# Performance work log

Measured on AMD Instinct MI355X. Metric: run time of the kernel, lower is better.

## Reference

```python
import jax, jax.numpy as jnp
import numpy as np

D_MODEL = 256
NUM_HEAD = 4
D_HEAD = D_MODEL // NUM_HEAD
B, N, M = 1, 512, 512


def setup_inputs() -> dict:
    key = jax.random.key(0)
    ks = jax.random.split(key, 13)
    s = 1.0 / np.sqrt(D_MODEL)
    inp = {
        'input_q': jax.random.normal(ks[0], (B, N, D_MODEL), jnp.float32),
        'input_k': jax.random.normal(ks[1], (B, M, D_MODEL), jnp.float32),
        'input_v': jax.random.normal(ks[2], (B, M, D_MODEL), jnp.float32),
        'input_p': jax.random.normal(ks[3], (B, N, M, D_MODEL), jnp.float32),
        'key_masks': jnp.zeros((B, M), dtype=bool),
        'Wq': jax.random.normal(ks[4], (D_MODEL, D_MODEL), jnp.float32) * s,
        'bq': jnp.zeros((D_MODEL,), jnp.float32),
        'Wk': jax.random.normal(ks[5], (D_MODEL, D_MODEL), jnp.float32) * s,
        'bk': jnp.zeros((D_MODEL,), jnp.float32),
        'Wv': jax.random.normal(ks[6], (D_MODEL, D_MODEL), jnp.float32) * s,
        'bv': jnp.zeros((D_MODEL,), jnp.float32),
        'Wp': jax.random.normal(ks[7], (D_MODEL, D_MODEL), jnp.float32) * s,
        'bp': jnp.zeros((D_MODEL,), jnp.float32),
    }
    return inp


def reference(input_q, input_k, input_v, input_p, key_masks,
              Wq, bq, Wk, bk, Wv, bv, Wp, bp):
    H, Dh = NUM_HEAD, D_HEAD
    b, n, _ = input_q.shape
    m = input_k.shape[1]
    # linear projections (PyTorch Linear: x @ W.T + b)
    q = (input_q @ Wq.T + bq).reshape(b, n, H, Dh).transpose(0, 2, 1, 3)   # (B,H,N,Dh)
    k = (input_k @ Wk.T + bk).reshape(b, m, H, Dh).transpose(0, 2, 1, 3)   # (B,H,M,Dh)
    v = (input_v @ Wv.T + bv).reshape(b, m, H, Dh).transpose(0, 2, 1, 3)   # (B,H,M,Dh)
    p = (input_p @ Wp.T + bp).reshape(b, n, m, H, Dh)                      # (B,N,M,H,Dh)
    # content scores + per-pair RPE scores (q dot p)
    scores = (jnp.einsum('bhnd,bhmd->bhnm', q, k)
              + jnp.einsum('bhnd,bnmhd->bhnm', q, p)) / np.sqrt(Dh)
    scores = jnp.where(key_masks[:, None, None, :], -jnp.inf, scores)
    attn = jax.nn.softmax(scores, axis=-1)                                 # (B,H,N,M)
    hidden = jnp.einsum('bhnm,bhmd->bhnd', attn, v)
    hidden = hidden.transpose(0, 2, 1, 3).reshape(b, n, H * Dh)            # (B,N,C)
    return hidden
```

## Files before the change

### kernel.cpp

```cpp
#include <hip/hip_runtime.h>
#include <math.h>

#define DMODEL 256
#define NSEQ   512
#define MSEQ   512
#define NHEAD  4
#define DHEAD  64

#define WS_Q      0
#define WS_K      131072
#define WS_V      262144
#define WS_WPE    393216
#define WS_SCORES 917504

__global__ __launch_bounds__(256) void proj_qkv(
    const float* __restrict__ xq, const float* __restrict__ xk,
    const float* __restrict__ xv,
    const float* __restrict__ Wq, const float* __restrict__ bq,
    const float* __restrict__ Wk, const float* __restrict__ bk,
    const float* __restrict__ Wv, const float* __restrict__ bv,
    float* __restrict__ ws)
{
    int bid = blockIdx.x;
    int mat = bid >> 6;
    int rb  = bid & 63;
    const float* X; const float* W; const float* b; float* Y;
    if (mat == 0)      { X = xq; W = Wq; b = bq; Y = ws + WS_Q; }
    else if (mat == 1) { X = xk; W = Wk; b = bk; Y = ws + WS_K; }
    else               { X = xv; W = Wv; b = bv; Y = ws + WS_V; }

    int c  = threadIdx.x;
    int r0 = rb * 8;
    float acc[8];
    float bias = b[c];
#pragma unroll
    for (int r = 0; r < 8; ++r) acc[r] = bias;

    const float4* Wrow = (const float4*)(W + (size_t)c * DMODEL);
    for (int d4 = 0; d4 < 64; ++d4) {
        float4 w = Wrow[d4];
#pragma unroll
        for (int r = 0; r < 8; ++r) {
            float4 x = ((const float4*)(X + (size_t)(r0 + r) * DMODEL))[d4];
            acc[r] += w.x * x.x + w.y * x.y + w.z * x.z + w.w * x.w;
        }
    }
#pragma unroll
    for (int r = 0; r < 8; ++r)
        Y[(size_t)(r0 + r) * DMODEL + c] = acc[r];
}

__global__ __launch_bounds__(256) void make_wpeff(
    const float* __restrict__ Wp, float* __restrict__ ws)
{
    const float* q   = ws + WS_Q;
    float*       wpe = ws + WS_WPE;
    int n0 = blockIdx.x * 2;
    int d  = threadIdx.x;

    const float* q0 = q + (size_t)n0 * DMODEL;
    const float* q1 = q0 + DMODEL;

    float acc0[4] = {0.f, 0.f, 0.f, 0.f};
    float acc1[4] = {0.f, 0.f, 0.f, 0.f};
#pragma unroll
    for (int h = 0; h < 4; ++h) {
        for (int dh = 0; dh < 64; ++dh) {
            int c = h * 64 + dh;
            float w = Wp[(size_t)c * DMODEL + d];
            acc0[h] += q0[c] * w;
            acc1[h] += q1[c] * w;
        }
    }
    *(float4*)&wpe[(size_t)n0 * 1024 + d * 4] =
        make_float4(acc0[0], acc0[1], acc0[2], acc0[3]);
    *(float4*)&wpe[(size_t)(n0 + 1) * 1024 + d * 4] =
        make_float4(acc1[0], acc1[1], acc1[2], acc1[3]);
}

__global__ __launch_bounds__(256) void p_scores(
    const float* __restrict__ Xp, float* __restrict__ ws)
{
    const float* wpe    = ws + WS_WPE;
    float*       scores = ws + WS_SCORES;

    int bid  = blockIdx.x;
    int n    = bid >> 1;
    int half = bid & 1;
    int m    = half * 256 + threadIdx.x;

    __shared__ float4 wl[256];
    wl[threadIdx.x] = ((const float4*)(wpe + (size_t)n * 1024))[threadIdx.x];
    __syncthreads();

    const float4* xrow =
        (const float4*)(Xp + (size_t)((size_t)n * MSEQ + m) * DMODEL);
    float4 acc = make_float4(0.f, 0.f, 0.f, 0.f);
#pragma unroll 8
    for (int d4 = 0; d4 < 64; ++d4) {
        float4 x  = xrow[d4];
        float4 w0 = wl[d4 * 4 + 0];
        float4 w1 = wl[d4 * 4 + 1];
        float4 w2 = wl[d4 * 4 + 2];
        float4 w3 = wl[d4 * 4 + 3];
        acc.x += x.x * w0.x + x.y * w1.x + x.z * w2.x + x.w * w3.x;
        acc.y += x.x * w0.y + x.y * w1.y + x.z * w2.y + x.w * w3.y;
        acc.z += x.x * w0.z + x.y * w1.z + x.z * w2.z + x.w * w3.z;
        acc.w += x.x * w0.w + x.y * w1.w + x.z * w2.w + x.w * w3.w;
    }
    size_t base = (size_t)n * MSEQ + m;
    scores[0 * 262144 + base] = acc.x;
    scores[1 * 262144 + base] = acc.y;
    scores[2 * 262144 + base] = acc.z;
    scores[3 * 262144 + base] = acc.w;
}

__global__ __launch_bounds__(256) void qk_scores(
    const float* __restrict__ bp, float* __restrict__ ws)
{
    const float* q      = ws + WS_Q;
    const float* k      = ws + WS_K;
    float*       scores = ws + WS_SCORES;

    int bid = blockIdx.x;
    int h   = bid >> 6;
    int nt  = (bid >> 3) & 7;
    int mt  = bid & 7;
    int n0  = nt * 64, m0 = mt * 64;

    __shared__ float qs[64][76];
    __shared__ float ks[64][76];
    __shared__ float qb[64];

    int tid = threadIdx.x;
#pragma unroll
    for (int rep = 0; rep < 4; ++rep) {
        int idx = rep * 1024 + tid * 4;
        int row = idx >> 6, col = idx & 63;
        *(float4*)&qs[row][col] =
            *(const float4*)&q[(size_t)(n0 + row) * DMODEL + h * 64 + col];
        *(float4*)&ks[row][col] =
            *(const float4*)&k[(size_t)(m0 + row) * DMODEL + h * 64 + col];
    }
    __syncthreads();

    if (tid < 64) {
        float s = 0.f;
        for (int dh = 0; dh < 64; ++dh) s += qs[tid][dh] * bp[h * 64 + dh];
        qb[tid] = s;
    }
    __syncthreads();

    int tn = tid >> 4, tm = tid & 15;
    float acc[4][4] = {};
    for (int kk = 0; kk < 64; kk += 4) {
        float4 qf[4], kf[4];
#pragma unroll
        for (int i = 0; i < 4; ++i) {
            qf[i] = *(const float4*)&qs[tn * 4 + i][kk];
            kf[i] = *(const float4*)&ks[tm * 4 + i][kk];
        }
#pragma unroll
        for (int i = 0; i < 4; ++i)
#pragma unroll
            for (int j = 0; j < 4; ++j)
                acc[i][j] += qf[i].x * kf[j].x + qf[i].y * kf[j].y +
                             qf[i].z * kf[j].z + qf[i].w * kf[j].w;
    }

#pragma unroll
    for (int i = 0; i < 4; ++i) {
        int n = n0 + tn * 4 + i;
        float qbn = qb[tn * 4 + i];
        float4* p = (float4*)&scores[(size_t)h * 262144 +
                                     (size_t)n * MSEQ + m0 + tm * 4];
        float4 sp = *p;
        sp.x = 0.125f * (sp.x + acc[i][0] + qbn);
        sp.y = 0.125f * (sp.y + acc[i][1] + qbn);
        sp.z = 0.125f * (sp.z + acc[i][2] + qbn);
        sp.w = 0.125f * (sp.w + acc[i][3] + qbn);
        *p = sp;
    }
}

__global__ __launch_bounds__(256) void softmax_av(
    const unsigned char* __restrict__ mask,
    float* __restrict__ out, float* __restrict__ ws)
{
    const float* v      = ws + WS_V;
    const float* scores = ws + WS_SCORES;

    int bid = blockIdx.x;
    int h   = bid >> 6;
    int g   = bid & 63;
    int n0  = g * 8;

    __shared__ float  pl[MSEQ * 8];
    __shared__ float4 red4[256];
    __shared__ float  wred[4];

    int tid  = threadIdx.x;
    int lane = tid & 63, wv = tid >> 6;

    for (int j = 0; j < 8; ++j) {
        int n = n0 + j;
        const float* srow = scores + (size_t)h * 262144 + (size_t)n * MSEQ;
        float s0 = srow[tid];
        float s1 = srow[tid + 256];
        if (mask[tid])       s0 = -INFINITY;
        if (mask[tid + 256]) s1 = -INFINITY;

        float mx = fmaxf(s0, s1);
#pragma unroll
        for (int off = 32; off; off >>= 1) mx = fmaxf(mx, __shfl_xor(mx, off));
        if (lane == 0) wred[wv] = mx;
        __syncthreads();
        mx = fmaxf(fmaxf(wred[0], wred[1]), fmaxf(wred[2], wred[3]));

        float e0 = __expf(s0 - mx);
        float e1 = __expf(s1 - mx);
        float sm = e0 + e1;
#pragma unroll
        for (int off = 32; off; off >>= 1) sm += __shfl_xor(sm, off);
        __syncthreads();
        if (lane == 0) wred[wv] = sm;
        __syncthreads();
        sm = wred[0] + wred[1] + wred[2] + wred[3];
        float rinv = 1.0f / sm;

        pl[(size_t)tid * 8 + j]         = e0 * rinv;
        pl[(size_t)(tid + 256) * 8 + j] = e1 * rinv;
        __syncthreads();
    }

    int dhq = tid & 15, mq = tid >> 4;
    float acc[8][4] = {};
    for (int i = 0; i < 32; ++i) {
        int m = mq * 32 + i;
        float4 vv = *(const float4*)&v[(size_t)m * DMODEL + h * 64 + dhq * 4];
        float4 pa = *(const float4*)&pl[m * 8];
        float4 pb = *(const float4*)&pl[m * 8 + 4];
#pragma unroll
        for (int j = 0; j < 4; ++j) {
            float p = (&pa.x)[j];
            acc[j][0] += p * vv.x; acc[j][1] += p * vv.y;
            acc[j][2] += p * vv.z; acc[j][3] += p * vv.w;
        }
#pragma unroll
        for (int j = 0; j < 4; ++j) {
            float p = (&pb.x)[j];
            acc[4 + j][0] += p * vv.x; acc[4 + j][1] += p * vv.y;
            acc[4 + j][2] += p * vv.z; acc[4 + j][3] += p * vv.w;
        }
    }

    for (int j = 0; j < 8; ++j) {
        red4[mq * 16 + dhq] =
            make_float4(acc[j][0], acc[j][1], acc[j][2], acc[j][3]);
        __syncthreads();
        if (tid < 64) {
            int dq = tid >> 2, x = tid & 3;
            float s = 0.f;
#pragma unroll
            for (int qq = 0; qq < 16; ++qq)
                s += ((const float*)&red4[qq * 16 + dq])[x];
            out[(size_t)(n0 + j) * DMODEL + h * 64 + tid] = s;
        }
        __syncthreads();
    }
}

extern "C" void kernel_launch(void* const* d_in, const int* in_sizes, int n_in,
                              void* d_out, int out_size, void* d_ws,
                              size_t ws_size, hipStream_t stream)
{
    const float* xq = (const float*)d_in[0];
    const float* xk = (const float*)d_in[1];
    const float* xv = (const float*)d_in[2];
    const float* xp = (const float*)d_in[3];
    const unsigned char* mask = (const unsigned char*)d_in[4];
    const float* Wq = (const float*)d_in[5];
    const float* bq = (const float*)d_in[6];
    const float* Wk = (const float*)d_in[7];
    const float* bk = (const float*)d_in[8];
    const float* Wv = (const float*)d_in[9];
    const float* bv = (const float*)d_in[10];
    const float* Wp = (const float*)d_in[11];
    const float* bp = (const float*)d_in[12];
    float* out = (float*)d_out;
    float* ws  = (float*)d_ws;

    proj_qkv  <<<192,  256, 0, stream>>>(xq, xk, xv, Wq, bq, Wk, bk, Wv, bv, ws);
    make_wpeff<<<256,  256, 0, stream>>>(Wp, ws);
    p_scores  <<<1024, 256, 0, stream>>>(xp, ws);
    qk_scores <<<256,  256, 0, stream>>>(bp, ws);
    softmax_av<<<256,  256, 0, stream>>>(mask, out, ws);
}
```

Before: 102.7 us.

## Coalesce input_p reads in p_scores with cooperative lanes and shuffle reduction

p_scores previously had each thread stream its own 1KB row of input_p, so every lane in a wave read a different row. Now 16 lanes share one row and read contiguous float4 chunks, with the projected weights held in registers. Partial dot products are reduced with xor shuffles and staged through LDS for coalesced score writes. Separately, softmax_av pads its probability buffer to stride 9 and interleaves the m index across thread groups to reduce LDS bank conflicts, but the float4 LDS reads at stride 9 are no longer 16-byte aligned.

```diff
diff --git a/kernel.cpp b/kernel.cpp
--- a/kernel.cpp
+++ b/kernel.cpp
@@ -86,33 +86,70 @@
 
     int bid  = blockIdx.x;
     int n    = bid >> 1;
-    int half = bid & 1;
-    int m    = half * 256 + threadIdx.x;
-
-    __shared__ float4 wl[256];
-    wl[threadIdx.x] = ((const float4*)(wpe + (size_t)n * 1024))[threadIdx.x];
+    int m0   = (bid & 1) * 256;
+    int tid  = threadIdx.x;
+    int wv   = tid >> 6;
+    int lane = tid & 63;
+    int p    = lane & 15;
+    int r3   = lane >> 4;
+
+    const float4* wp4 = (const float4*)(wpe + (size_t)n * 1024);
+    float4 w[4][4];
+#pragma unroll
+    for (int j = 0; j < 4; ++j)
+#pragma unroll
+        for (int c = 0; c < 4; ++c)
+            w[j][c] = wp4[4 * p + 64 * j + c];
+
+    __shared__ float sm[4][256];
+
+    const float4* base4 =
+        (const float4*)Xp + ((size_t)n * MSEQ + m0 + wv * 64) * 64;
+
+#pragma unroll 2
+    for (int g = 0; g < 16; ++g) {
+        int rbase = (g * 4 + r3) * 64 + p;
+        float4 xv0 = base4[rbase + 0];
+        float4 xv1 = base4[rbase + 16];
+        float4 xv2 = base4[rbase + 32];
+        float4 xv3 = base4[rbase + 48];
+
+        float sh[4] = {0.f, 0.f, 0.f, 0.f};
+        {
+            const float4 xs[4] = {xv0, xv1, xv2, xv3};
+#pragma unroll
+            for (int j = 0; j < 4; ++j) {
+                const float* xc = &xs[j].x;
+#pragma unroll
+                for (int c = 0; c < 4; ++c) {
+                    const float* wf = &w[j][c].x;
+#pragma unroll
+                    for (int h = 0; h < 4; ++h)
+                        sh[h] += xc[c] * wf[h];
+                }
+            }
+        }
+#pragma unroll
+        for (int off = 1; off < 16; off <<= 1) {
+#pragma unroll
+            for (int h = 0; h < 4; ++h)
+                sh[h] += __shfl_xor(sh[h], off);
+        }
+        if (p == 0) {
+            int ml = wv * 64 + g * 4 + r3;
+            sm[0][ml] = sh[0];
+            sm[1][ml] = sh[1];
+            sm[2][ml] = sh[2];
+            sm[3][ml] = sh[3];
+        }
+    }
     __syncthreads();
 
-    const float4* xrow =
-        (const float4*)(Xp + (size_t)((size_t)n * MSEQ + m) * DMODEL);
-    float4 acc = make_float4(0.f, 0.f, 0.f, 0.f);
-#pragma unroll 8
-    for (int d4 = 0; d4 < 64; ++d4) {
-        float4 x  = xrow[d4];
-        float4 w0 = wl[d4 * 4 + 0];
-        float4 w1 = wl[d4 * 4 + 1];
-        float4 w2 = wl[d4 * 4 + 2];
-        float4 w3 = wl[d4 * 4 + 3];
-        acc.x += x.x * w0.x + x.y * w1.x + x.z * w2.x + x.w * w3.x;
-        acc.y += x.x * w0.y + x.y * w1.y + x.z * w2.y + x.w * w3.y;
-        acc.z += x.x * w0.z + x.y * w1.z + x.z * w2.z + x.w * w3.z;
-        acc.w += x.x * w0.w + x.y * w1.w + x.z * w2.w + x.w * w3.w;
-    }
-    size_t base = (size_t)n * MSEQ + m;
-    scores[0 * 262144 + base] = acc.x;
-    scores[1 * 262144 + base] = acc.y;
-    scores[2 * 262144 + base] = acc.z;
-    scores[3 * 262144 + base] = acc.w;
+    size_t ob = (size_t)n * MSEQ + m0 + tid;
+    scores[0 * 262144 + ob] = sm[0][tid];
+    scores[1 * 262144 + ob] = sm[1][tid];
+    scores[2 * 262144 + ob] = sm[2][tid];
+    scores[3 * 262144 + ob] = sm[3][tid];
 }
 
 __global__ __launch_bounds__(256) void qk_scores(
@@ -172,14 +209,14 @@
     for (int i = 0; i < 4; ++i) {
         int n = n0 + tn * 4 + i;
         float qbn = qb[tn * 4 + i];
-        float4* p = (float4*)&scores[(size_t)h * 262144 +
-                                     (size_t)n * MSEQ + m0 + tm * 4];
-        float4 sp = *p;
+        float4* pp = (float4*)&scores[(size_t)h * 262144 +
+                                      (size_t)n * MSEQ + m0 + tm * 4];
+        float4 sp = *pp;
         sp.x = 0.125f * (sp.x + acc[i][0] + qbn);
         sp.y = 0.125f * (sp.y + acc[i][1] + qbn);
         sp.z = 0.125f * (sp.z + acc[i][2] + qbn);
         sp.w = 0.125f * (sp.w + acc[i][3] + qbn);
-        *p = sp;
+        *pp = sp;
     }
 }
 
@@ -195,7 +232,7 @@
     int g   = bid & 63;
     int n0  = g * 8;
 
-    __shared__ float  pl[MSEQ * 8];
+    __shared__ float  pl[MSEQ * 9];
     __shared__ float4 red4[256];
     __shared__ float  wred[4];
 
@@ -228,29 +265,29 @@
         sm = wred[0] + wred[1] + wred[2] + wred[3];
         float rinv = 1.0f / sm;
 
-        pl[(size_t)tid * 8 + j]         = e0 * rinv;
-        pl[(size_t)(tid + 256) * 8 + j] = e1 * rinv;
+        pl[(size_t)tid * 9 + j]         = e0 * rinv;
+        pl[(size_t)(tid + 256) * 9 + j] = e1 * rinv;
         __syncthreads();
     }
 
     int dhq = tid & 15, mq = tid >> 4;
     float acc[8][4] = {};
     for (int i = 0; i < 32; ++i) {
-        int m = mq * 32 + i;
+        int m = i * 16 + mq;
         float4 vv = *(const float4*)&v[(size_t)m * DMODEL + h * 64 + dhq * 4];
-        float4 pa = *(const float4*)&pl[m * 8];
-        float4 pb = *(const float4*)&pl[m * 8 + 4];
+        float4 pa = *(const float4*)&pl[(size_t)m * 9];
+        float4 pb = *(const float4*)&pl[(size_t)m * 9 + 4];
 #pragma unroll
         for (int j = 0; j < 4; ++j) {
-            float p = (&pa.x)[j];
-            acc[j][0] += p * vv.x; acc[j][1] += p * vv.y;
-            acc[j][2] += p * vv.z; acc[j][3] += p * vv.w;
+            float pv = (&pa.x)[j];
+            acc[j][0] += pv * vv.x; acc[j][1] += pv * vv.y;
+            acc[j][2] += pv * vv.z; acc[j][3] += pv * vv.w;
         }
 #pragma unroll
         for (int j = 0; j < 4; ++j) {
-            float p = (&pb.x)[j];
-            acc[4 + j][0] += p * vv.x; acc[4 + j][1] += p * vv.y;
-            acc[4 + j][2] += p * vv.z; acc[4 + j][3] += p * vv.w;
+            float pv = (&pb.x)[j];
+            acc[4 + j][0] += pv * vv.x; acc[4 + j][1] += pv * vv.y;
+            acc[4 + j][2] += pv * vv.z; acc[4 + j][3] += pv * vv.w;
         }
     }
 
```

Measured after the change: 108.1 us. 1.05x slower.

## Fuse RPE score, softmax and AV into one per-query-row kernel

Applied to the files above, without the earlier changes.

Replaces the separate p_scores and softmax_av kernels with a single fused_attn kernel that, per query row, streams input_p with nontemporal loads, adds precomputed QK scores, does a four-head softmax in registers and shared memory, and multiplies by V. The QK scores kernel now writes pre-scaled scores instead of read-modify-writing the RPE scores, and make_wpeff processes one row per block from shared memory. This removes a full score-buffer write and reread plus one launch. In exchange the AV product now rereads V from global per row with strided loads.

```diff
diff --git a/kernel.cpp b/kernel.cpp
--- a/kernel.cpp
+++ b/kernel.cpp
@@ -4,14 +4,14 @@
 #define DMODEL 256
 #define NSEQ   512
 #define MSEQ   512
-#define NHEAD  4
-#define DHEAD  64
 
 #define WS_Q      0
 #define WS_K      131072
 #define WS_V      262144
 #define WS_WPE    393216
-#define WS_SCORES 917504
+#define WS_SQK    917504
+
+typedef float v4f __attribute__((ext_vector_type(4)));
 
 __global__ __launch_bounds__(256) void proj_qkv(
     const float* __restrict__ xq, const float* __restrict__ xk,
@@ -55,219 +55,175 @@
 {
     const float* q   = ws + WS_Q;
     float*       wpe = ws + WS_WPE;
-    int n0 = blockIdx.x * 2;
-    int d  = threadIdx.x;
-
-    const float* q0 = q + (size_t)n0 * DMODEL;
-    const float* q1 = q0 + DMODEL;
-
-    float acc0[4] = {0.f, 0.f, 0.f, 0.f};
-    float acc1[4] = {0.f, 0.f, 0.f, 0.f};
+    int n = blockIdx.x;
+    int d = threadIdx.x;
+
+    __shared__ float ql[256];
+    ql[d] = q[(size_t)n * DMODEL + d];
+    __syncthreads();
+
+    float acc[4];
 #pragma unroll
     for (int h = 0; h < 4; ++h) {
+        float a = 0.f;
+#pragma unroll 8
         for (int dh = 0; dh < 64; ++dh) {
             int c = h * 64 + dh;
-            float w = Wp[(size_t)c * DMODEL + d];
-            acc0[h] += q0[c] * w;
-            acc1[h] += q1[c] * w;
+            a += ql[c] * Wp[(size_t)c * DMODEL + d];
         }
-    }
-    *(float4*)&wpe[(size_t)n0 * 1024 + d * 4] =
-        make_float4(acc0[0], acc0[1], acc0[2], acc0[3]);
-    *(float4*)&wpe[(size_t)(n0 + 1) * 1024 + d * 4] =
-        make_float4(acc1[0], acc1[1], acc1[2], acc1[3]);
-}
-
-__global__ __launch_bounds__(256) void p_scores(
-    const float* __restrict__ Xp, float* __restrict__ ws)
-{
-    const float* wpe    = ws + WS_WPE;
-    float*       scores = ws + WS_SCORES;
-
-    int bid  = blockIdx.x;
-    int n    = bid >> 1;
-    int half = bid & 1;
-    int m    = half * 256 + threadIdx.x;
+        acc[h] = a;
+    }
+    *(float4*)&wpe[(size_t)n * 1024 + d * 4] =
+        make_float4(acc[0], acc[1], acc[2], acc[3]);
+}
+
+__global__ __launch_bounds__(256) void qk_scores(
+    const float* __restrict__ bp, float* __restrict__ ws)
+{
+    const float* q   = ws + WS_Q;
+    const float* k   = ws + WS_K;
+    float*       sqk = ws + WS_SQK;
+
+    int bid = blockIdx.x;
+    int h   = bid >> 6;
+    int g   = bid & 63;
+    int n0  = g * 8;
+    int tid = threadIdx.x;
+
+    __shared__ float qls[8][64];
+    __shared__ float qb[8];
+
+    if (tid < 128) {
+        int row = tid >> 4, col = (tid & 15) * 4;
+        *(float4*)&qls[row][col] =
+            *(const float4*)&q[(size_t)(n0 + row) * DMODEL + h * 64 + col];
+    }
+    __syncthreads();
+    if (tid < 8) {
+        float s = 0.f;
+        for (int dh = 0; dh < 64; ++dh) s += qls[tid][dh] * bp[h * 64 + dh];
+        qb[tid] = s;
+    }
+    __syncthreads();
+
+    const float* ka = k + (size_t)tid * DMODEL + h * 64;
+    const float* kb = ka + (size_t)256 * DMODEL;
+    float acca[8] = {};
+    float accb[8] = {};
+#pragma unroll 4
+    for (int d4 = 0; d4 < 16; ++d4) {
+        float4 xa = *(const float4*)(ka + d4 * 4);
+        float4 xb = *(const float4*)(kb + d4 * 4);
+#pragma unroll
+        for (int j = 0; j < 8; ++j) {
+            float4 qq = *(const float4*)&qls[j][d4 * 4];
+            acca[j] += xa.x * qq.x + xa.y * qq.y + xa.z * qq.z + xa.w * qq.w;
+            accb[j] += xb.x * qq.x + xb.y * qq.y + xb.z * qq.z + xb.w * qq.w;
+        }
+    }
+#pragma unroll
+    for (int j = 0; j < 8; ++j) {
+        size_t base = (size_t)h * 262144 + (size_t)(n0 + j) * MSEQ;
+        sqk[base + tid]       = 0.125f * (acca[j] + qb[j]);
+        sqk[base + tid + 256] = 0.125f * (accb[j] + qb[j]);
+    }
+}
+
+__global__ __launch_bounds__(512) void fused_attn(
+    const float* __restrict__ Xp, const unsigned char* __restrict__ mask,
+    float* __restrict__ out, float* __restrict__ ws)
+{
+    const float* wpe = ws + WS_WPE;
+    const float* v   = ws + WS_V;
+    const float* sqk = ws + WS_SQK;
+
+    int n    = blockIdx.x;
+    int tid  = threadIdx.x;
+    int lane = tid & 63, wv = tid >> 6;
 
     __shared__ float4 wl[256];
-    wl[threadIdx.x] = ((const float4*)(wpe + (size_t)n * 1024))[threadIdx.x];
-    __syncthreads();
-
-    const float4* xrow =
-        (const float4*)(Xp + (size_t)((size_t)n * MSEQ + m) * DMODEL);
-    float4 acc = make_float4(0.f, 0.f, 0.f, 0.f);
+    __shared__ float4 sc[512];
+    __shared__ float4 wredm[8];
+    __shared__ float4 wreds[8];
+    __shared__ float  red[256];
+
+    if (tid < 256)
+        wl[tid] = *(const float4*)&wpe[(size_t)n * 1024 + tid * 4];
+    __syncthreads();
+
+    const v4f* xrow = (const v4f*)(Xp + ((size_t)n * MSEQ + tid) * DMODEL);
+    float s0 = 0.f, s1 = 0.f, s2 = 0.f, s3 = 0.f;
 #pragma unroll 8
     for (int d4 = 0; d4 < 64; ++d4) {
-        float4 x  = xrow[d4];
+        v4f x = __builtin_nontemporal_load(&xrow[d4]);
         float4 w0 = wl[d4 * 4 + 0];
         float4 w1 = wl[d4 * 4 + 1];
         float4 w2 = wl[d4 * 4 + 2];
         float4 w3 = wl[d4 * 4 + 3];
-        acc.x += x.x * w0.x + x.y * w1.x + x.z * w2.x + x.w * w3.x;
-        acc.y += x.x * w0.y + x.y * w1.y + x.z * w2.y + x.w * w3.y;
-        acc.z += x.x * w0.z + x.y * w1.z + x.z * w2.z + x.w * w3.z;
-        acc.w += x.x * w0.w + x.y * w1.w + x.z * w2.w + x.w * w3.w;
-    }
-    size_t base = (size_t)n * MSEQ + m;
-    scores[0 * 262144 + base] = acc.x;
-    scores[1 * 262144 + base] = acc.y;
-    scores[2 * 262144 + base] = acc.z;
-    scores[3 * 262144 + base] = acc.w;
-}
-
-__global__ __launch_bounds__(256) void qk_scores(
-    const float* __restrict__ bp, float* __restrict__ ws)
-{
-    const float* q      = ws + WS_Q;
-    const float* k      = ws + WS_K;
-    float*       scores = ws + WS_SCORES;
-
-    int bid = blockIdx.x;
-    int h   = bid >> 6;
-    int nt  = (bid >> 3) & 7;
-    int mt  = bid & 7;
-    int n0  = nt * 64, m0 = mt * 64;
-
-    __shared__ float qs[64][76];
-    __shared__ float ks[64][76];
-    __shared__ float qb[64];
-
-    int tid = threadIdx.x;
-#pragma unroll
-    for (int rep = 0; rep < 4; ++rep) {
-        int idx = rep * 1024 + tid * 4;
-        int row = idx >> 6, col = idx & 63;
-        *(float4*)&qs[row][col] =
-            *(const float4*)&q[(size_t)(n0 + row) * DMODEL + h * 64 + col];
-        *(float4*)&ks[row][col] =
-            *(const float4*)&k[(size_t)(m0 + row) * DMODEL + h * 64 + col];
-    }
-    __syncthreads();
-
-    if (tid < 64) {
-        float s = 0.f;
-        for (int dh = 0; dh < 64; ++dh) s += qs[tid][dh] * bp[h * 64 + dh];
-        qb[tid] = s;
-    }
-    __syncthreads();
-
-    int tn = tid >> 4, tm = tid & 15;
-    float acc[4][4] = {};
-    for (int kk = 0; kk < 64; kk += 4) {
-        float4 qf[4], kf[4];
-#pragma unroll
-        for (int i = 0; i < 4; ++i) {
-            qf[i] = *(const float4*)&qs[tn * 4 + i][kk];
-            kf[i] = *(const float4*)&ks[tm * 4 + i][kk];
-        }
-#pragma unroll
-        for (int i = 0; i < 4; ++i)
-#pragma unroll
-            for (int j = 0; j < 4; ++j)
-                acc[i][j] += qf[i].x * kf[j].x + qf[i].y * kf[j].y +
-                             qf[i].z * kf[j].z + qf[i].w * kf[j].w;
-    }
-
-#pragma unroll
-    for (int i = 0; i < 4; ++i) {
-        int n = n0 + tn * 4 + i;
-        float qbn = qb[tn * 4 + i];
-        float4* p = (float4*)&scores[(size_t)h * 262144 +
-                                     (size_t)n * MSEQ + m0 + tm * 4];
-        float4 sp = *p;
-        sp.x = 0.125f * (sp.x + acc[i][0] + qbn);
-        sp.y = 0.125f * (sp.y + acc[i][1] + qbn);
-        sp.z = 0.125f * (sp.z + acc[i][2] + qbn);
-        sp.w = 0.125f * (sp.w + acc[i][3] + qbn);
-        *p = sp;
-    }
-}
-
-__global__ __launch_bounds__(256) void softmax_av(
-    const unsigned char* __restrict__ mask,
-    float* __restrict__ out, float* __restrict__ ws)
-{
-    const float* v      = ws + WS_V;
-    const float* scores = ws + WS_SCORES;
-
-    int bid = blockIdx.x;
-    int h   = bid >> 6;
-    int g   = bid & 63;
-    int n0  = g * 8;
-
-    __shared__ float  pl[MSEQ * 8];
-    __shared__ float4 red4[256];
-    __shared__ float  wred[4];
-
-    int tid  = threadIdx.x;
-    int lane = tid & 63, wv = tid >> 6;
-
-    for (int j = 0; j < 8; ++j) {
-        int n = n0 + j;
-        const float* srow = scores + (size_t)h * 262144 + (size_t)n * MSEQ;
-        float s0 = srow[tid];
-        float s1 = srow[tid + 256];
-        if (mask[tid])       s0 = -INFINITY;
-        if (mask[tid + 256]) s1 = -INFINITY;
-
-        float mx = fmaxf(s0, s1);
-#pragma unroll
-        for (int off = 32; off; off >>= 1) mx = fmaxf(mx, __shfl_xor(mx, off));
-        if (lane == 0) wred[wv] = mx;
-        __syncthreads();
-        mx = fmaxf(fmaxf(wred[0], wred[1]), fmaxf(wred[2], wred[3]));
-
-        float e0 = __expf(s0 - mx);
-        float e1 = __expf(s1 - mx);
-        float sm = e0 + e1;
-#pragma unroll
-        for (int off = 32; off; off >>= 1) sm += __shfl_xor(sm, off);
-        __syncthreads();
-        if (lane == 0) wred[wv] = sm;
-        __syncthreads();
-        sm = wred[0] + wred[1] + wred[2] + wred[3];
-        float rinv = 1.0f / sm;
-
-        pl[(size_t)tid * 8 + j]         = e0 * rinv;
-        pl[(size_t)(tid + 256) * 8 + j] = e1 * rinv;
-        __syncthreads();
-    }
-
-    int dhq = tid & 15, mq = tid >> 4;
-    float acc[8][4] = {};
-    for (int i = 0; i < 32; ++i) {
-        int m = mq * 32 + i;
-        float4 vv = *(const float4*)&v[(size_t)m * DMODEL + h * 64 + dhq * 4];
-        float4 pa = *(const float4*)&pl[m * 8];
-        float4 pb = *(const float4*)&pl[m * 8 + 4];
-#pragma unroll
-        for (int j = 0; j < 4; ++j) {
-            float p = (&pa.x)[j];
-            acc[j][0] += p * vv.x; acc[j][1] += p * vv.y;
-            acc[j][2] += p * vv.z; acc[j][3] += p * vv.w;
-        }
-#pragma unroll
-        for (int j = 0; j < 4; ++j) {
-            float p = (&pb.x)[j];
-            acc[4 + j][0] += p * vv.x; acc[4 + j][1] += p * vv.y;
-            acc[4 + j][2] += p * vv.z; acc[4 + j][3] += p * vv.w;
-        }
-    }
-
-    for (int j = 0; j < 8; ++j) {
-        red4[mq * 16 + dhq] =
-            make_float4(acc[j][0], acc[j][1], acc[j][2], acc[j][3]);
-        __syncthreads();
-        if (tid < 64) {
-            int dq = tid >> 2, x = tid & 3;
-            float s = 0.f;
-#pragma unroll
-            for (int qq = 0; qq < 16; ++qq)
-                s += ((const float*)&red4[qq * 16 + dq])[x];
-            out[(size_t)(n0 + j) * DMODEL + h * 64 + tid] = s;
-        }
-        __syncthreads();
-    }
+        s0 += x.x * w0.x + x.y * w1.x + x.z * w2.x + x.w * w3.x;
+        s1 += x.x * w0.y + x.y * w1.y + x.z * w2.y + x.w * w3.y;
+        s2 += x.x * w0.z + x.y * w1.z + x.z * w2.z + x.w * w3.z;
+        s3 += x.x * w0.w + x.y * w1.w + x.z * w2.w + x.w * w3.w;
+    }
+
+    size_t ob = (size_t)n * MSEQ + tid;
+    float s[4];
+    s[0] = sqk[0 * 262144 + ob] + 0.125f * s0;
+    s[1] = sqk[1 * 262144 + ob] + 0.125f * s1;
+    s[2] = sqk[2 * 262144 + ob] + 0.125f * s2;
+    s[3] = sqk[3 * 262144 + ob] + 0.125f * s3;
+    if (mask[tid]) { s[0] = s[1] = s[2] = s[3] = -INFINITY; }
+
+    float mx[4] = { s[0], s[1], s[2], s[3] };
+#pragma unroll
+    for (int off = 32; off; off >>= 1) {
+#pragma unroll
+        for (int h = 0; h < 4; ++h) mx[h] = fmaxf(mx[h], __shfl_xor(mx[h], off));
+    }
+    if (lane == 0) wredm[wv] = make_float4(mx[0], mx[1], mx[2], mx[3]);
+    __syncthreads();
+    float4 M = wredm[0];
+#pragma unroll
+    for (int w = 1; w < 8; ++w) {
+        float4 t = wredm[w];
+        M.x = fmaxf(M.x, t.x); M.y = fmaxf(M.y, t.y);
+        M.z = fmaxf(M.z, t.z); M.w = fmaxf(M.w, t.w);
+    }
+
+    float e[4];
+    e[0] = __expf(s[0] - M.x); e[1] = __expf(s[1] - M.y);
+    e[2] = __expf(s[2] - M.z); e[3] = __expf(s[3] - M.w);
+    float sm[4] = { e[0], e[1], e[2], e[3] };
+#pragma unroll
+    for (int off = 32; off; off >>= 1) {
+#pragma unroll
+        for (int h = 0; h < 4; ++h) sm[h] += __shfl_xor(sm[h], off);
+    }
+    if (lane == 0) wreds[wv] = make_float4(sm[0], sm[1], sm[2], sm[3]);
+    __syncthreads();
+    float4 S = wreds[0];
+#pragma unroll
+    for (int w = 1; w < 8; ++w) {
+        float4 t = wreds[w];
+        S.x += t.x; S.y += t.y; S.z += t.z; S.w += t.w;
+    }
+
+    sc[tid] = make_float4(e[0] * (1.f / S.x), e[1] * (1.f / S.y),
+                          e[2] * (1.f / S.z), e[3] * (1.f / S.w));
+    __syncthreads();
+
+    int c = tid & 255, half = tid >> 8;
+    int hh = c >> 6;
+    const float* vcol = v + c;
+    float acc = 0.f;
+#pragma unroll 8
+    for (int i = 0; i < 256; ++i) {
+        int m = half * 256 + i;
+        acc += ((const float*)&sc[m])[hh] * vcol[(size_t)m * DMODEL];
+    }
+    if (half) red[c] = acc;
+    __syncthreads();
+    if (!half) out[(size_t)n * DMODEL + c] = acc + red[c];
 }
 
 extern "C" void kernel_launch(void* const* d_in, const int* in_sizes, int n_in,
@@ -290,9 +246,8 @@
     float* out = (float*)d_out;
     float* ws  = (float*)d_ws;
 
-    proj_qkv  <<<192,  256, 0, stream>>>(xq, xk, xv, Wq, bq, Wk, bk, Wv, bv, ws);
-    make_wpeff<<<256,  256, 0, stream>>>(Wp, ws);
-    p_scores  <<<1024, 256, 0, stream>>>(xp, ws);
-    qk_scores <<<256,  256, 0, stream>>>(bp, ws);
-    softmax_av<<<256,  256, 0, stream>>>(mask, out, ws);
-}
+    proj_qkv  <<<192, 256, 0, stream>>>(xq, xk, xv, Wq, bq, Wk, bk, Wv, bv, ws);
+    make_wpeff<<<512, 256, 0, stream>>>(Wp, ws);
+    qk_scores <<<256, 256, 0, stream>>>(bp, ws);
+    fused_attn<<<512, 512, 0, stream>>>(xp, mask, out, ws);
+}
```

New measurement: 173.5 us. 1.69x slower.
